# Kernel tuning notes

Measured on AMD Instinct MI355X. Metric: run time of the kernel, lower is better.

The kernel has to match this reference:

```python
import jax, jax.numpy as jnp
import numpy as np

BN_EPS = 1e-5


def setup_inputs() -> dict:
    key = jax.random.key(0)
    ks = jax.random.split(key, 8)
    B, C, H, W = 8, 256, 64, 64
    Ci = 128
    x = jax.random.normal(ks[0], (B, C, H, W), dtype=jnp.float32)
    # 1x1 conv weights stored as [out, in] (kernel size 1 squeezed)
    sc = 1.0 / np.sqrt(C)
    g_w = jax.random.uniform(ks[1], (Ci, C), jnp.float32, -sc, sc)
    g_b = jax.random.uniform(ks[2], (Ci,), jnp.float32, -sc, sc)
    theta_w = jax.random.uniform(ks[3], (Ci, C), jnp.float32, -sc, sc)
    theta_b = jax.random.uniform(ks[4], (Ci,), jnp.float32, -sc, sc)
    phi_w = jax.random.uniform(ks[5], (Ci, C), jnp.float32, -sc, sc)
    phi_b = jax.random.uniform(ks[6], (Ci,), jnp.float32, -sc, sc)
    # W conv: normal(std=0.01) weight, zero bias (per _init_weights)
    W_w = 0.01 * jax.random.normal(ks[7], (C, Ci), dtype=jnp.float32)
    W_b = jnp.zeros((C,), dtype=jnp.float32)
    bn_gamma = jnp.ones((C,), dtype=jnp.float32)
    bn_beta = jnp.zeros((C,), dtype=jnp.float32)
    return {"x": x, "g_w": g_w, "g_b": g_b, "theta_w": theta_w, "theta_b": theta_b,
            "phi_w": phi_w, "phi_b": phi_b, "W_w": W_w, "W_b": W_b,
            "bn_gamma": bn_gamma, "bn_beta": bn_beta}


def reference(x, g_w, g_b, theta_w, theta_b, phi_w, phi_b, W_w, W_b, bn_gamma, bn_beta):
    B, C, H, W = x.shape
    xf = x.reshape(B, C, H * W)                                   # [B, C, N]
    # 1x1 convs == per-position channel GEMMs
    g_x = jnp.einsum('oc,bcn->bon', g_w, xf) + g_b[:, None]        # [B, Ci, N]
    th = jnp.einsum('oc,bcn->bon', theta_w, xf) + theta_b[:, None]
    ph = jnp.einsum('oc,bcn->bon', phi_w, xf) + phi_b[:, None]
    # theta^T phi : [B, N, N] dense attention scores
    f = jnp.einsum('bcn,bcm->bnm', th, ph)
    attn = jax.nn.softmax(f, axis=-1)
    # attention-weighted sum of g values -> [B, Ci, N]
    y = jnp.einsum('bnm,bcm->bcn', attn, g_x)
    # output 1x1 conv + BatchNorm2d (training-mode batch stats)
    wy = jnp.einsum('oc,bcn->bon', W_w, y) + W_b[:, None]          # [B, C, N]
    mean = jnp.mean(wy, axis=(0, 2), keepdims=True)
    var = jnp.var(wy, axis=(0, 2), keepdims=True)
    wy_bn = (wy - mean) * jax.lax.rsqrt(var + BN_EPS)
    wy_bn = wy_bn * bn_gamma[:, None] + bn_beta[:, None]
    z = wy_bn.reshape(B, C, H, W) + x
    return z
```

## Files before the change

### kernel.cpp

```cpp
#include <hip/hip_runtime.h>
#include <hip/hip_bf16.h>
#include <math.h>

#define B_   8
#define C_   256
#define CI_  128
#define N_   4096

typedef unsigned short ushort_t;
typedef unsigned int uint_t;
typedef __attribute__((ext_vector_type(8))) short short8;
typedef __attribute__((ext_vector_type(16))) float floatx16;
typedef __attribute__((ext_vector_type(2))) unsigned int uint2v;

#define OFF_W3B  0ull
#define OFF_B3   196608ull
#define OFF_WCB  198144ull
#define OFF_XT   263680ull
#define OFF_THT  17040896ull
#define OFF_PHT  25429504ull
#define OFF_G16  33818112ull
#define OFF_LP   42206720ull
#define OFF_YPB  42468864ull
#define OFF_WY   263680ull
#define OFF_ST   59246080ull

__device__ __forceinline__ ushort_t f2bf(float x) {
  union { float f; uint_t u; } c; c.f = x;
  return (ushort_t)((c.u + 0x7fffu + ((c.u >> 16) & 1u)) >> 16);
}
__device__ __forceinline__ uint_t pkbf(float a, float b) {
  __hip_bfloat162 h = __float22bfloat162_rn(float2{a, b});
  union { __hip_bfloat162 h; uint_t u; } c; c.h = h; return c.u;
}
__device__ __forceinline__ float bf_lo(uint_t u) {
  union { uint_t u; float f; } c; c.u = u << 16; return c.f;
}
__device__ __forceinline__ float bf_hi(uint_t u) {
  union { uint_t u; float f; } c; c.u = u & 0xffff0000u; return c.f;
}
__device__ __forceinline__ void async_copy16(const void* g, void* l) {
  __builtin_amdgcn_global_load_lds(
      (const __attribute__((address_space(1))) unsigned int*)g,
      (__attribute__((address_space(3))) unsigned int*)l, 16, 0, 0);
}

__global__ __launch_bounds__(256) void pack_w(
    const float* __restrict__ g_w, const float* __restrict__ g_b,
    const float* __restrict__ th_w, const float* __restrict__ th_b,
    const float* __restrict__ ph_w, const float* __restrict__ ph_b,
    const float* __restrict__ W_w,
    ushort_t* __restrict__ W3b, float* __restrict__ b3,
    ushort_t* __restrict__ Wc)
{
  int bid = blockIdx.x;
  if (bid < 384) {
    int i = bid * 256 + threadIdx.x;
    int o = i >> 8;
    float v;
    if (o < 128)      v = g_w[i];
    else if (o < 256) v = th_w[i - 128*256];
    else              v = ph_w[i - 256*256];
    W3b[i] = f2bf(v);
    if ((i & 255) == 0)
      b3[o] = (o < 128) ? g_b[o] : (o < 256) ? th_b[o - 128] : ph_b[o - 256];
  } else {
    int j = (bid - 384) * 256 + threadIdx.x;
    Wc[j] = f2bf(W_w[j]);
  }
}

__global__ __launch_bounds__(256) void xcast(
    const float* __restrict__ x, ushort_t* __restrict__ xt)
{
  const int b = blockIdx.z, c0 = blockIdx.y * 64, n0 = blockIdx.x * 64;
  const int tid = threadIdx.x;
  __shared__ float xs[64][65];
  const int nq = (tid & 15) * 4, cr = tid >> 4;
  #pragma unroll
  for (int i = 0; i < 4; ++i) {
    float4 v = *(const float4*)&x[((size_t)b * C_ + c0 + cr + 16*i) * N_ + n0 + nq];
    xs[cr + 16*i][nq] = v.x; xs[cr + 16*i][nq+1] = v.y;
    xs[cr + 16*i][nq+2] = v.z; xs[cr + 16*i][nq+3] = v.w;
  }
  __syncthreads();
  const int n = tid >> 2, cs = (tid & 3) * 16;
  uint_t u[8];
  #pragma unroll
  for (int j = 0; j < 8; ++j)
    u[j] = pkbf(xs[cs + 2*j][n], xs[cs + 2*j + 1][n]);
  ushort_t* dst = &xt[((size_t)b * N_ + n0 + n) * C_ + c0 + cs];
  *(uint4*)dst       = make_uint4(u[0], u[1], u[2], u[3]);
  *(uint4*)(dst + 8) = make_uint4(u[4], u[5], u[6], u[7]);
}

__global__ __launch_bounds__(256, 2) void proj_all(
    const ushort_t* __restrict__ W3b, const float* __restrict__ b3,
    const ushort_t* __restrict__ xt, ushort_t* __restrict__ tht,
    ushort_t* __restrict__ pht, ushort_t* __restrict__ g16)
{
  const int b = blockIdx.z, nb = blockIdx.x, ot = blockIdx.y;
  const int gm = (ot == 2);
  const int o0 = gm ? 0 : (128 + ot * 128);
  const int tid = threadIdx.x, w = tid >> 6, lane = tid & 63;
  const int l31 = lane & 31, h = lane >> 5, xk = l31 & 7;
  __shared__ ushort_t ws_l[128 * 64];
  __shared__ ushort_t xs_l[128 * 64];
  const ushort_t* xb = xt + (size_t)b * N_ * C_;
  const int n0 = nb * 128;
  floatx16 acc[4];
  #pragma unroll
  for (int ct = 0; ct < 4; ++ct)
    #pragma unroll
    for (int r = 0; r < 16; ++r) acc[ct][r] = 0.f;

  const int gr = lane >> 3, gu = lane & 7;
  for (int k0 = 0; k0 < C_; k0 += 64) {
    __syncthreads();
    #pragma unroll
    for (int i = 0; i < 4; ++i) {
      int r = w*32 + i*8 + gr;
      async_copy16(&W3b[(size_t)(o0 + r) * C_ + k0 + ((gu ^ (r & 7)) * 8)],
                   &ws_l[(w*32 + i*8) * 64]);
      async_copy16(&xb[(size_t)(n0 + r) * C_ + k0 + ((gu ^ (r & 7)) * 8)],
                   &xs_l[(w*32 + i*8) * 64]);
    }
    __syncthreads();
    const ushort_t* bmat = gm ? ws_l : xs_l;
    const ushort_t* amat = gm ? xs_l : ws_l;
    #pragma unroll
    for (int kk = 0; kk < 4; ++kk) {
      int fc = ((2*kk + h) ^ xk) * 8;
      short8 bf = *(const short8*)&bmat[(w*32 + l31) * 64 + fc];
      #pragma unroll
      for (int ct = 0; ct < 4; ++ct) {
        short8 af = *(const short8*)&amat[(ct*32 + l31) * 64 + fc];
        acc[ct] = __builtin_amdgcn_mfma_f32_32x32x16_bf16(af, bf, acc[ct], 0, 0, 0);
      }
    }
  }

  if (gm) {
    float bv = b3[w*32 + l31];
    ushort_t* gp = g16 + ((size_t)b * CI_ + w*32 + l31) * N_;
    #pragma unroll
    for (int ct = 0; ct < 4; ++ct)
      #pragma unroll
      for (int rq = 0; rq < 4; ++rq) {
        uint2 d = make_uint2(pkbf(acc[ct][4*rq+0] + bv, acc[ct][4*rq+1] + bv),
                             pkbf(acc[ct][4*rq+2] + bv, acc[ct][4*rq+3] + bv));
        *(uint2*)&gp[n0 + ct*32 + 8*rq + 4*h] = d;
      }
  } else {
    ushort_t* tp = ((ot == 0) ? tht : pht) + ((size_t)b * N_ + n0 + w*32 + l31) * CI_;
    #pragma unroll
    for (int ct = 0; ct < 4; ++ct)
      #pragma unroll
      for (int rq = 0; rq < 4; ++rq) {
        float4 bv = *(const float4*)&b3[o0 + ct*32 + 8*rq + 4*h];
        uint2 d = make_uint2(pkbf(acc[ct][4*rq+0] + bv.x, acc[ct][4*rq+1] + bv.y),
                             pkbf(acc[ct][4*rq+2] + bv.z, acc[ct][4*rq+3] + bv.w));
        *(uint2*)&tp[ct*32 + 8*rq + 4*h] = d;
      }
  }
}

#define LOG2E_  1.442695041f
#define MBIAS_  (-28.85390082f)

__global__ __launch_bounds__(256, 2) void attn_mfma(
    const ushort_t* __restrict__ tht, const ushort_t* __restrict__ pht,
    const ushort_t* __restrict__ g16, ushort_t* __restrict__ yp,
    float* __restrict__ lp)
{
  const int b  = blockIdx.x & 7;
  const int ms = (blockIdx.x >> 3) & 1;
  const int qb = blockIdx.x >> 4;
  const int tid = threadIdx.x, w = tid >> 6, lane = tid & 63;
  const int l31 = lane & 31, h = lane >> 5, xk = l31 & 7;

  __shared__ ushort_t smem[32768];

  const int q0w = qb * 128 + w * 32;
  const int m_base = ms * 2048;

  const ushort_t* thb = tht + (size_t)b * N_ * CI_;
  const ushort_t* phb = pht + (size_t)b * N_ * CI_;
  const ushort_t* gbp = g16 + (size_t)b * CI_ * N_;

  short8 tf[8];
  #pragma unroll
  for (int kk = 0; kk < 8; ++kk)
    tf[kk] = *(const short8*)&thb[(size_t)(q0w + l31) * CI_ + kk*16 + h*8];

  floatx16 acc[4];
  #pragma unroll
  for (int ct = 0; ct < 4; ++ct)
    #pragma unroll
    for (int r = 0; r < 16; ++r) acc[ct][r] = 0.f;
  float lpart = 0.f;

  const int phr = lane >> 4, phu = lane & 15;
  const int gr  = lane >> 3, gu  = lane & 7;

  #define STAGE_ATTN(m0v, bufv)                                               \
    {                                                                         \
      ushort_t* phs_ = smem + (bufv) * 8192;                                  \
      ushort_t* gs_  = smem + 16384 + (bufv) * 8192;                          \
      _Pragma("unroll")                                                       \
      for (int i = 0; i < 4; ++i) {                                           \
        int row = w*16 + i*4 + phr;                                           \
        async_copy16(&phb[(size_t)((m0v) + row) * CI_ + ((phu ^ (row & 7)) * 8)], \
                     &phs_[(w*16 + i*4) * 128]);                              \
      }                                                                       \
      _Pragma("unroll")                                                       \
      for (int i = 0; i < 4; ++i) {                                           \
        int c = w*32 + i*8 + gr;                                              \
        async_copy16(&gbp[(size_t)c * N_ + (m0v) + ((gu ^ (c & 7)) * 8)],     \
                     &gs_[(w*32 + i*8) * 64]);                                \
      }                                                                       \
    }

  #define SMPV(sv, mtv)                                                       \
    {                                                                         \
      uint_t Aw[4], Bw[4];                                                    \
      float ls = 0.f;                                                         \
      _Pragma("unroll")                                                       \
      for (int rq = 0; rq < 4; ++rq) {                                        \
        float p0 = exp2f(fmaf(sv[4*rq+0], LOG2E_, MBIAS_));                   \
        float p1 = exp2f(fmaf(sv[4*rq+1], LOG2E_, MBIAS_));                   \
        float p2 = exp2f(fmaf(sv[4*rq+2], LOG2E_, MBIAS_));                   \
        float p3 = exp2f(fmaf(sv[4*rq+3], LOG2E_, MBIAS_));                   \
        ls += (p0 + p1) + (p2 + p3);                                          \
        Aw[rq] = pkbf(p0, p1);                                                \
        Bw[rq] = pkbf(p2, p3);                                                \
      }                                                                       \
      lpart += ls;                                                            \
      _Pragma("unroll")                                                       \
      for (int t = 0; t < 2; ++t) {                                           \
        uint2v ra = __builtin_amdgcn_permlane32_swap(Aw[2*t], Aw[2*t+1], false, false); \
        uint2v rb = __builtin_amdgcn_permlane32_swap(Bw[2*t], Bw[2*t+1], false, false); \
        union { uint_t u[4]; short8 s; } pk_;                                 \
        pk_.u[0] = ra.x; pk_.u[1] = rb.x; pk_.u[2] = ra.y; pk_.u[3] = rb.y;   \
        const int pc = ((2*(2*(mtv) + t) + h) ^ xk) * 8;                      \
        __builtin_amdgcn_s_setprio(1);                                        \
        _Pragma("unroll")                                                     \
        for (int ct = 0; ct < 4; ++ct) {                                      \
          short8 gf = *(const short8*)&gs[(ct*32 + l31) * 64 + pc];           \
          acc[ct] = __builtin_amdgcn_mfma_f32_32x32x16_bf16(gf, pk_.s, acc[ct], 0, 0, 0); \
        }                                                                     \
        __builtin_amdgcn_s_setprio(0);                                        \
      }                                                                       \
    }

  STAGE_ATTN(m_base, 0);
  asm volatile("s_waitcnt vmcnt(0)" ::: "memory");
  __builtin_amdgcn_s_barrier();

  #pragma unroll 2
  for (int it = 0; it < 32; ++it) {
    const int cur = it & 1;
    const int m0 = m_base + it * 64;
    if (it < 31) STAGE_ATTN(m0 + 64, cur ^ 1);
    const ushort_t* phs = smem + cur * 8192;
    const ushort_t* gs  = smem + 16384 + cur * 8192;

    floatx16 s0, s1;
    #pragma unroll
    for (int r = 0; r < 16; ++r) { s0[r] = 0.f; s1[r] = 0.f; }
    __builtin_amdgcn_s_setprio(1);
    #pragma unroll
    for (int kk = 0; kk < 8; ++kk) {
      const int fc = (((2*kk + h) ^ xk) * 8);
      short8 pf0 = *(const short8*)&phs[(l31) * 128 + fc];
      s0 = __builtin_amdgcn_mfma_f32_32x32x16_bf16(pf0, tf[kk], s0, 0, 0, 0);
      short8 pf1 = *(const short8*)&phs[(32 + l31) * 128 + fc];
      s1 = __builtin_amdgcn_mfma_f32_32x32x16_bf16(pf1, tf[kk], s1, 0, 0, 0);
    }
    __builtin_amdgcn_s_setprio(0);

    SMPV(s0, 0)
    SMPV(s1, 1)

    asm volatile("s_waitcnt vmcnt(0)" ::: "memory");
    __builtin_amdgcn_s_barrier();
  }

  float lq = lpart + __shfl_xor(lpart, 32);
  if (h == 0)
    lp[((size_t)ms * 8 + b) * N_ + q0w + l31] = lq;

  __syncthreads();
  ushort_t* tr = smem + w * 4096;
  #pragma unroll
  for (int ct = 0; ct < 4; ++ct)
    #pragma unroll
    for (int rq = 0; rq < 4; ++rq) {
      uint2 d = make_uint2(pkbf(acc[ct][4*rq+0], acc[ct][4*rq+1]),
                           pkbf(acc[ct][4*rq+2], acc[ct][4*rq+3]));
      *(uint2*)&tr[l31 * 128 + ct*32 + 8*rq + 4*h] = d;
    }
  ushort_t* ypb = yp + (((size_t)ms * 8 + b) * N_ + q0w) * CI_;
  #pragma unroll
  for (int itx = 0; itx < 8; ++itx) {
    int row = itx*4 + (lane >> 4);
    int cu  = (lane & 15) * 8;
    uint4 v = *(const uint4*)&tr[row * 128 + cu];
    *(uint4*)&ypb[(size_t)row * CI_ + cu] = v;
  }
}

__global__ __launch_bounds__(256, 2) void wgemm_fused(
    const ushort_t* __restrict__ Wc, const float* __restrict__ Wb,
    const ushort_t* __restrict__ yp, const float* __restrict__ lp,
    float* __restrict__ WY)
{
  const int b = blockIdx.z, nb = blockIdx.x, ot = blockIdx.y;
  const int o0 = ot * 128;
  const int tid = threadIdx.x, w = tid >> 6, lane = tid & 63;
  const int l31 = lane & 31, h = lane >> 5, xk = l31 & 7;
  __shared__ ushort_t ws_l[128 * 64];
  __shared__ ushort_t xs_l[128 * 64];
  const int n0 = nb * 128;
  const size_t PH = (size_t)B_ * N_ * CI_;
  const ushort_t* yp0 = yp + (size_t)b * N_ * CI_;
  const ushort_t* yp1 = yp0 + PH;
  floatx16 acc[4];
  #pragma unroll
  for (int ct = 0; ct < 4; ++ct)
    #pragma unroll
    for (int r = 0; r < 16; ++r) acc[ct][r] = 0.f;

  const int gr = lane >> 3, gu = lane & 7;
  for (int k0 = 0; k0 < CI_; k0 += 64) {
    __syncthreads();
    #pragma unroll
    for (int i = 0; i < 4; ++i) {
      int r = w*32 + i*8 + gr;
      async_copy16(&Wc[(size_t)(o0 + r) * CI_ + k0 + ((gu ^ (r & 7)) * 8)],
                   &ws_l[(w*32 + i*8) * 64]);
      int n = n0 + r;
      size_t src = (size_t)n * CI_ + k0 + ((gu ^ (r & 7)) * 8);
      uint4 a0 = *(const uint4*)&yp0[src];
      uint4 a1 = *(const uint4*)&yp1[src];
      float inv = 1.0f / (lp[(size_t)b * N_ + n] + lp[(size_t)(8 + b) * N_ + n]);
      uint4 o;
      o.x = pkbf((bf_lo(a0.x) + bf_lo(a1.x)) * inv, (bf_hi(a0.x) + bf_hi(a1.x)) * inv);
      o.y = pkbf((bf_lo(a0.y) + bf_lo(a1.y)) * inv, (bf_hi(a0.y) + bf_hi(a1.y)) * inv);
      o.z = pkbf((bf_lo(a0.z) + bf_lo(a1.z)) * inv, (bf_hi(a0.z) + bf_hi(a1.z)) * inv);
      o.w = pkbf((bf_lo(a0.w) + bf_lo(a1.w)) * inv, (bf_hi(a0.w) + bf_hi(a1.w)) * inv);
      *(uint4*)&xs_l[r * 64 + gu * 8] = o;
    }
    __syncthreads();
    #pragma unroll
    for (int kk = 0; kk < 4; ++kk) {
      int fc = ((2*kk + h) ^ xk) * 8;
      short8 bf = *(const short8*)&xs_l[(w*32 + l31) * 64 + fc];
      #pragma unroll
      for (int ct = 0; ct < 4; ++ct) {
        short8 af = *(const short8*)&ws_l[(ct*32 + l31) * 64 + fc];
        acc[ct] = __builtin_amdgcn_mfma_f32_32x32x16_bf16(af, bf, acc[ct], 0, 0, 0);
      }
    }
  }
  const int n = n0 + w*32 + l31;
  #pragma unroll
  for (int ct = 0; ct < 4; ++ct)
    #pragma unroll
    for (int rq = 0; rq < 4; ++rq) {
      float4 bv = *(const float4*)&Wb[o0 + ct*32 + 8*rq + 4*h];
      #pragma unroll
      for (int j = 0; j < 4; ++j) {
        int o = o0 + ct*32 + 8*rq + 4*h + j;
        WY[((size_t)b * C_ + o) * N_ + n] = acc[ct][4*rq + j] + (&bv.x)[j];
      }
    }
}

__global__ __launch_bounds__(256) void bn_stats(
    const float* __restrict__ WY, float* __restrict__ st)
{
  const int o = blockIdx.x;
  const int tid = threadIdx.x;
  float s = 0.f, s2 = 0.f;
  for (int b = 0; b < B_; ++b) {
    const float* p = WY + ((size_t)b * C_ + o) * N_;
    for (int n = tid * 4; n < N_; n += 256 * 4) {
      float4 v = *(const float4*)&p[n];
      s  += v.x + v.y + v.z + v.w;
      s2 += v.x * v.x + v.y * v.y + v.z * v.z + v.w * v.w;
    }
  }
  __shared__ float rs[256], rs2[256];
  rs[tid] = s; rs2[tid] = s2;
  __syncthreads();
  for (int off = 128; off > 0; off >>= 1) {
    if (tid < off) { rs[tid] += rs[tid + off]; rs2[tid] += rs2[tid + off]; }
    __syncthreads();
  }
  if (tid == 0) {
    const float M = (float)(B_ * N_);
    float mean = rs[0] / M;
    float var  = rs2[0] / M - mean * mean;
    st[o] = mean;
    st[256 + o] = rsqrtf(var + 1e-5f);
  }
}

__global__ __launch_bounds__(256) void bn_apply(
    const float* __restrict__ WY, const float* __restrict__ x,
    const float* __restrict__ st, const float* __restrict__ gamma,
    const float* __restrict__ beta, float* __restrict__ out)
{
  size_t i = ((size_t)blockIdx.x * 256 + threadIdx.x) * 4;
  int o = (int)((i >> 12) & 255);
  float4 w  = *(const float4*)&WY[i];
  float4 xv = *(const float4*)&x[i];
  float gsc = gamma[o] * st[256 + o];
  float bb  = beta[o] - st[o] * gsc;
  float4 v;
  v.x = w.x * gsc + bb + xv.x;
  v.y = w.y * gsc + bb + xv.y;
  v.z = w.z * gsc + bb + xv.z;
  v.w = w.w * gsc + bb + xv.w;
  *(float4*)&out[i] = v;
}

extern "C" void kernel_launch(void* const* d_in, const int* in_sizes, int n_in,
                              void* d_out, int out_size, void* d_ws, size_t ws_size,
                              hipStream_t stream)
{
  const float* x       = (const float*)d_in[0];
  const float* g_w     = (const float*)d_in[1];
  const float* g_b     = (const float*)d_in[2];
  const float* theta_w = (const float*)d_in[3];
  const float* theta_b = (const float*)d_in[4];
  const float* phi_w   = (const float*)d_in[5];
  const float* phi_b   = (const float*)d_in[6];
  const float* W_w     = (const float*)d_in[7];
  const float* W_b     = (const float*)d_in[8];
  const float* gamma   = (const float*)d_in[9];
  const float* beta    = (const float*)d_in[10];
  float* out = (float*)d_out;

  char* ws = (char*)d_ws;
  ushort_t* W3b = (ushort_t*)(ws + OFF_W3B);
  float*    b3  = (float*)(ws + OFF_B3);
  ushort_t* Wc  = (ushort_t*)(ws + OFF_WCB);
  ushort_t* xt  = (ushort_t*)(ws + OFF_XT);
  ushort_t* tht = (ushort_t*)(ws + OFF_THT);
  ushort_t* pht = (ushort_t*)(ws + OFF_PHT);
  ushort_t* g16 = (ushort_t*)(ws + OFF_G16);
  float*    lpp = (float*)(ws + OFF_LP);
  ushort_t* ypb = (ushort_t*)(ws + OFF_YPB);
  float*    WY  = (float*)(ws + OFF_WY);
  float*    ST  = (float*)(ws + OFF_ST);

  pack_w<<<512, 256, 0, stream>>>(g_w, g_b, theta_w, theta_b, phi_w, phi_b,
                                  W_w, W3b, b3, Wc);
  xcast<<<dim3(64, 4, 8), 256, 0, stream>>>(x, xt);
  proj_all<<<dim3(32, 3, 8), 256, 0, stream>>>(W3b, b3, xt, tht, pht, g16);
  attn_mfma<<<512, 256, 0, stream>>>(tht, pht, g16, ypb, lpp);
  wgemm_fused<<<dim3(32, 2, 8), 256, 0, stream>>>(Wc, W_b, ypb, lpp, WY);
  bn_stats<<<256, 256, 0, stream>>>(WY, ST);
  bn_apply<<<8192, 256, 0, stream>>>(WY, x, ST, gamma, beta, out);
}
```

Baseline: 253.0 us.

## Single-buffer G tile for occupancy, use raw v_exp, store WY as bf16

The attention kernel now keeps only one G tile in LDS, shrinking shared memory from 64KB to 48KB, and raises launch bounds to 3 blocks per CU. The softmax probabilities for all four key sub-tiles are packed first, then a mid-iteration barrier waits for the G load before the PV MFMAs run. exp2f is replaced by an inline v_exp_f32. Separately, the pre-BatchNorm output WY is written as bf16 instead of fp32, halving the traffic in bn_stats and bn_apply at the cost of extra rounding before normalization. The extra barrier and the tighter register budget under 3 blocks per CU could hurt the attention loop.

```diff
diff --git a/kernel.cpp b/kernel.cpp
--- a/kernel.cpp
+++ b/kernel.cpp
@@ -38,6 +38,9 @@
 }
 __device__ __forceinline__ float bf_hi(uint_t u) {
   union { uint_t u; float f; } c; c.u = u & 0xffff0000u; return c.f;
+}
+__device__ __forceinline__ float fexp2(float x) {
+  float r; asm("v_exp_f32 %0, %1\ns_nop 0" : "=v"(r) : "v"(x)); return r;
 }
 __device__ __forceinline__ void async_copy16(const void* g, void* l) {
   __builtin_amdgcn_global_load_lds(
@@ -168,7 +171,7 @@
 #define LOG2E_  1.442695041f
 #define MBIAS_  (-28.85390082f)
 
-__global__ __launch_bounds__(256, 2) void attn_mfma(
+__global__ __launch_bounds__(256, 3) void attn_mfma(
     const ushort_t* __restrict__ tht, const ushort_t* __restrict__ pht,
     const ushort_t* __restrict__ g16, ushort_t* __restrict__ yp,
     float* __restrict__ lp)
@@ -179,7 +182,7 @@
   const int tid = threadIdx.x, w = tid >> 6, lane = tid & 63;
   const int l31 = lane & 31, h = lane >> 5, xk = l31 & 7;
 
-  __shared__ ushort_t smem[32768];
+  __shared__ ushort_t smem[24576];
 
   const int q0w = qb * 128 + w * 32;
   const int m_base = ms * 2048;
@@ -203,16 +206,19 @@
   const int phr = lane >> 4, phu = lane & 15;
   const int gr  = lane >> 3, gu  = lane & 7;
 
-  #define STAGE_ATTN(m0v, bufv)                                               \
+  #define STAGE_PHS(m0v, bufv)                                                \
     {                                                                         \
       ushort_t* phs_ = smem + (bufv) * 8192;                                  \
-      ushort_t* gs_  = smem + 16384 + (bufv) * 8192;                          \
       _Pragma("unroll")                                                       \
       for (int i = 0; i < 4; ++i) {                                           \
         int row = w*16 + i*4 + phr;                                           \
         async_copy16(&phb[(size_t)((m0v) + row) * CI_ + ((phu ^ (row & 7)) * 8)], \
                      &phs_[(w*16 + i*4) * 128]);                              \
       }                                                                       \
+    }
+  #define STAGE_GS(m0v)                                                       \
+    {                                                                         \
+      ushort_t* gs_ = smem + 16384;                                           \
       _Pragma("unroll")                                                       \
       for (int i = 0; i < 4; ++i) {                                           \
         int c = w*32 + i*8 + gr;                                              \
@@ -221,16 +227,16 @@
       }                                                                       \
     }
 
-  #define SMPV(sv, mtv)                                                       \
+  #define SMX(sv, base)                                                       \
     {                                                                         \
       uint_t Aw[4], Bw[4];                                                    \
       float ls = 0.f;                                                         \
       _Pragma("unroll")                                                       \
       for (int rq = 0; rq < 4; ++rq) {                                        \
-        float p0 = exp2f(fmaf(sv[4*rq+0], LOG2E_, MBIAS_));                   \
-        float p1 = exp2f(fmaf(sv[4*rq+1], LOG2E_, MBIAS_));                   \
-        float p2 = exp2f(fmaf(sv[4*rq+2], LOG2E_, MBIAS_));                   \
-        float p3 = exp2f(fmaf(sv[4*rq+3], LOG2E_, MBIAS_));                   \
+        float p0 = fexp2(fmaf(sv[4*rq+0], LOG2E_, MBIAS_));                   \
+        float p1 = fexp2(fmaf(sv[4*rq+1], LOG2E_, MBIAS_));                   \
+        float p2 = fexp2(fmaf(sv[4*rq+2], LOG2E_, MBIAS_));                   \
+        float p3 = fexp2(fmaf(sv[4*rq+3], LOG2E_, MBIAS_));                   \
         ls += (p0 + p1) + (p2 + p3);                                          \
         Aw[rq] = pkbf(p0, p1);                                                \
         Bw[rq] = pkbf(p2, p3);                                                \
@@ -242,28 +248,21 @@
         uint2v rb = __builtin_amdgcn_permlane32_swap(Bw[2*t], Bw[2*t+1], false, false); \
         union { uint_t u[4]; short8 s; } pk_;                                 \
         pk_.u[0] = ra.x; pk_.u[1] = rb.x; pk_.u[2] = ra.y; pk_.u[3] = rb.y;   \
-        const int pc = ((2*(2*(mtv) + t) + h) ^ xk) * 8;                      \
-        __builtin_amdgcn_s_setprio(1);                                        \
-        _Pragma("unroll")                                                     \
-        for (int ct = 0; ct < 4; ++ct) {                                      \
-          short8 gf = *(const short8*)&gs[(ct*32 + l31) * 64 + pc];           \
-          acc[ct] = __builtin_amdgcn_mfma_f32_32x32x16_bf16(gf, pk_.s, acc[ct], 0, 0, 0); \
-        }                                                                     \
-        __builtin_amdgcn_s_setprio(0);                                        \
+        pfrag[(base) + t] = pk_.s;                                            \
       }                                                                       \
     }
 
-  STAGE_ATTN(m_base, 0);
+  STAGE_PHS(m_base, 0);
   asm volatile("s_waitcnt vmcnt(0)" ::: "memory");
   __builtin_amdgcn_s_barrier();
 
-  #pragma unroll 2
   for (int it = 0; it < 32; ++it) {
     const int cur = it & 1;
     const int m0 = m_base + it * 64;
-    if (it < 31) STAGE_ATTN(m0 + 64, cur ^ 1);
+    STAGE_GS(m0);
+    if (it < 31) STAGE_PHS(m0 + 64, cur ^ 1);
     const ushort_t* phs = smem + cur * 8192;
-    const ushort_t* gs  = smem + 16384 + cur * 8192;
+    const ushort_t* gs  = smem + 16384;
 
     floatx16 s0, s1;
     #pragma unroll
@@ -279,8 +278,25 @@
     }
     __builtin_amdgcn_s_setprio(0);
 
-    SMPV(s0, 0)
-    SMPV(s1, 1)
+    short8 pfrag[4];
+    SMX(s0, 0)
+    SMX(s1, 2)
+
+    if (it < 31) { asm volatile("s_waitcnt vmcnt(4)" ::: "memory"); }
+    else         { asm volatile("s_waitcnt vmcnt(0)" ::: "memory"); }
+    __builtin_amdgcn_s_barrier();
+
+    __builtin_amdgcn_s_setprio(1);
+    #pragma unroll
+    for (int j = 0; j < 4; ++j) {
+      const int pc = (((2*j + h) ^ xk) * 8);
+      #pragma unroll
+      for (int ct = 0; ct < 4; ++ct) {
+        short8 gf = *(const short8*)&gs[(ct*32 + l31) * 64 + pc];
+        acc[ct] = __builtin_amdgcn_mfma_f32_32x32x16_bf16(gf, pfrag[j], acc[ct], 0, 0, 0);
+      }
+    }
+    __builtin_amdgcn_s_setprio(0);
 
     asm volatile("s_waitcnt vmcnt(0)" ::: "memory");
     __builtin_amdgcn_s_barrier();
@@ -313,7 +329,7 @@
 __global__ __launch_bounds__(256, 2) void wgemm_fused(
     const ushort_t* __restrict__ Wc, const float* __restrict__ Wb,
     const ushort_t* __restrict__ yp, const float* __restrict__ lp,
-    float* __restrict__ WY)
+    ushort_t* __restrict__ WYb)
 {
   const int b = blockIdx.z, nb = blockIdx.x, ot = blockIdx.y;
   const int o0 = ot * 128;
@@ -372,23 +388,25 @@
       #pragma unroll
       for (int j = 0; j < 4; ++j) {
         int o = o0 + ct*32 + 8*rq + 4*h + j;
-        WY[((size_t)b * C_ + o) * N_ + n] = acc[ct][4*rq + j] + (&bv.x)[j];
+        WYb[((size_t)b * C_ + o) * N_ + n] = f2bf(acc[ct][4*rq + j] + (&bv.x)[j]);
       }
     }
 }
 
 __global__ __launch_bounds__(256) void bn_stats(
-    const float* __restrict__ WY, float* __restrict__ st)
+    const ushort_t* __restrict__ WYb, float* __restrict__ st)
 {
   const int o = blockIdx.x;
   const int tid = threadIdx.x;
   float s = 0.f, s2 = 0.f;
   for (int b = 0; b < B_; ++b) {
-    const float* p = WY + ((size_t)b * C_ + o) * N_;
-    for (int n = tid * 4; n < N_; n += 256 * 4) {
-      float4 v = *(const float4*)&p[n];
-      s  += v.x + v.y + v.z + v.w;
-      s2 += v.x * v.x + v.y * v.y + v.z * v.z + v.w * v.w;
+    const ushort_t* p = WYb + ((size_t)b * C_ + o) * N_;
+    for (int n = tid * 8; n < N_; n += 256 * 8) {
+      uint4 v = *(const uint4*)&p[n];
+      float f0 = bf_lo(v.x), f1 = bf_hi(v.x), f2 = bf_lo(v.y), f3 = bf_hi(v.y);
+      float f4 = bf_lo(v.z), f5 = bf_hi(v.z), f6 = bf_lo(v.w), f7 = bf_hi(v.w);
+      s  += ((f0 + f1) + (f2 + f3)) + ((f4 + f5) + (f6 + f7));
+      s2 += ((f0*f0 + f1*f1) + (f2*f2 + f3*f3)) + ((f4*f4 + f5*f5) + (f6*f6 + f7*f7));
     }
   }
   __shared__ float rs[256], rs2[256];
@@ -408,21 +426,21 @@
 }
 
 __global__ __launch_bounds__(256) void bn_apply(
-    const float* __restrict__ WY, const float* __restrict__ x,
+    const ushort_t* __restrict__ WYb, const float* __restrict__ x,
     const float* __restrict__ st, const float* __restrict__ gamma,
     const float* __restrict__ beta, float* __restrict__ out)
 {
   size_t i = ((size_t)blockIdx.x * 256 + threadIdx.x) * 4;
   int o = (int)((i >> 12) & 255);
-  float4 w  = *(const float4*)&WY[i];
+  uint2 wv = *(const uint2*)&WYb[i];
   float4 xv = *(const float4*)&x[i];
   float gsc = gamma[o] * st[256 + o];
   float bb  = beta[o] - st[o] * gsc;
   float4 v;
-  v.x = w.x * gsc + bb + xv.x;
-  v.y = w.y * gsc + bb + xv.y;
-  v.z = w.z * gsc + bb + xv.z;
-  v.w = w.w * gsc + bb + xv.w;
+  v.x = bf_lo(wv.x) * gsc + bb + xv.x;
+  v.y = bf_hi(wv.x) * gsc + bb + xv.y;
+  v.z = bf_lo(wv.y) * gsc + bb + xv.z;
+  v.w = bf_hi(wv.y) * gsc + bb + xv.w;
   *(float4*)&out[i] = v;
 }
 
@@ -453,7 +471,7 @@
   ushort_t* g16 = (ushort_t*)(ws + OFF_G16);
   float*    lpp = (float*)(ws + OFF_LP);
   ushort_t* ypb = (ushort_t*)(ws + OFF_YPB);
-  float*    WY  = (float*)(ws + OFF_WY);
+  ushort_t* WYb = (ushort_t*)(ws + OFF_WY);
   float*    ST  = (float*)(ws + OFF_ST);
 
   pack_w<<<512, 256, 0, stream>>>(g_w, g_b, theta_w, theta_b, phi_w, phi_b,
@@ -461,7 +479,7 @@
   xcast<<<dim3(64, 4, 8), 256, 0, stream>>>(x, xt);
   proj_all<<<dim3(32, 3, 8), 256, 0, stream>>>(W3b, b3, xt, tht, pht, g16);
   attn_mfma<<<512, 256, 0, stream>>>(tht, pht, g16, ypb, lpp);
-  wgemm_fused<<<dim3(32, 2, 8), 256, 0, stream>>>(Wc, W_b, ypb, lpp, WY);
-  bn_stats<<<256, 256, 0, stream>>>(WY, ST);
-  bn_apply<<<8192, 256, 0, stream>>>(WY, x, ST, gamma, beta, out);
-}
+  wgemm_fused<<<dim3(32, 2, 8), 256, 0, stream>>>(Wc, W_b, ypb, lpp, WYb);
+  bn_stats<<<256, 256, 0, stream>>>(WYb, ST);
+  bn_apply<<<8192, 256, 0, stream>>>(WYb, x, ST, gamma, beta, out);
+}
```

Measured after the change: 412.4 us. 63.0% more time.
